# Optimization experiments

Hardware: AMD Instinct MI355X
Metric: run time of the kernel (lower is better)

The kernel has to match this reference:

```python
import jax, jax.numpy as jnp
import numpy as np

N_NODES = 50000
N_EDGES = 800000
C = 16          # in = hidden = out channels
FE = 8          # num_edge_features
NUM_GRAPHS = 64


def _nnconv(x, src, dst, edge_attr, w_e, b_e, root, bias):
    # edge MLP -> per-edge weight matrix [E, Cin, Cout]
    cin = x.shape[1]
    W = (edge_attr @ w_e + b_e).reshape(-1, cin, root.shape[1])
    msg = jnp.einsum('ei,eio->eo', x[src], W)            # gather + per-edge matvec
    n = x.shape[0]
    agg = jax.ops.segment_sum(msg, dst, num_segments=n)  # scatter-add
    cnt = jax.ops.segment_sum(jnp.ones((msg.shape[0], 1), x.dtype), dst, num_segments=n)
    agg = agg / jnp.maximum(cnt, 1.0)                    # aggr='mean'
    return x @ root + agg + bias


def setup_inputs() -> dict:
    key = jax.random.key(0)
    ks = jax.random.split(key, 12)
    x = jax.random.normal(ks[0], (N_NODES, C), dtype=jnp.float32)
    edge_index = jax.random.randint(ks[1], (2, N_EDGES), 0, N_NODES, dtype=jnp.int64)
    edge_attr = jax.random.uniform(ks[2], (N_EDGES, FE), dtype=jnp.float32)
    batch = jnp.sort(jax.random.randint(ks[3], (N_NODES,), 0, NUM_GRAPHS, dtype=jnp.int64))
    s = 1.0 / np.sqrt(C)
    se = 1.0 / np.sqrt(FE)
    we1 = jax.random.normal(ks[4], (FE, C * C), dtype=jnp.float32) * se
    be1 = jnp.zeros((C * C,), dtype=jnp.float32)
    root1 = jax.random.normal(ks[5], (C, C), dtype=jnp.float32) * s
    bias1 = jnp.zeros((C,), dtype=jnp.float32)
    we2 = jax.random.normal(ks[6], (FE, C * C), dtype=jnp.float32) * se
    be2 = jnp.zeros((C * C,), dtype=jnp.float32)
    root2 = jax.random.normal(ks[7], (C, C), dtype=jnp.float32) * s
    bias2 = jnp.zeros((C,), dtype=jnp.float32)
    return {"x": x, "edge_index": edge_index, "edge_attr": edge_attr, "batch": batch,
            "we1": we1, "be1": be1, "root1": root1, "bias1": bias1,
            "we2": we2, "be2": be2, "root2": root2, "bias2": bias2}


def reference(x, edge_index, edge_attr, batch,
              we1, be1, root1, bias1, we2, be2, root2, bias2):
    src, dst = edge_index[0], edge_index[1]
    # layer 1 (activation=None -> identity; dropout_prob=0 -> identity)
    h = _nnconv(x, src, dst, edge_attr, we1, be1, root1, bias1)
    # layer 2
    h = _nnconv(h, src, dst, edge_attr, we2, be2, root2, bias2)
    # global mean pool per graph, then flatten
    sums = jax.ops.segment_sum(h, batch, num_segments=NUM_GRAPHS)
    cnts = jax.ops.segment_sum(jnp.ones((h.shape[0], 1), h.dtype), batch, num_segments=NUM_GRAPHS)
    pooled = sums / jnp.maximum(cnts, 1.0)
    return pooled.reshape(-1)
```

## Files before the change

### kernel.cpp

```cpp
#include <hip/hip_runtime.h>

#define NN 50000
#define NE 800000
#define NG 64
#define NB ((NN + 255) / 256)
#define WSTR 164

__global__ __launch_bounds__(256) void histk(const int* __restrict__ dst,
                                             int* __restrict__ deg) {
    int e = blockIdx.x * 256 + threadIdx.x;
    if (e < NE) atomicAdd(&deg[dst[e]], 1);
}

__global__ __launch_bounds__(256) void bsumk(const int* __restrict__ deg,
                                             int* __restrict__ bsum) {
    int idx = blockIdx.x * 256 + threadIdx.x;
    int v = (idx < NN) ? deg[idx] : 0;
#pragma unroll
    for (int off = 32; off > 0; off >>= 1) v += __shfl_down(v, off);
    __shared__ int ws[4];
    int lane = threadIdx.x & 63, w = threadIdx.x >> 6;
    if (lane == 0) ws[w] = v;
    __syncthreads();
    if (threadIdx.x == 0) bsum[blockIdx.x] = ws[0] + ws[1] + ws[2] + ws[3];
}

__global__ __launch_bounds__(256) void bscank(const int* __restrict__ bsum,
                                              int* __restrict__ boffs) {
    int tid = threadIdx.x;
    int v = (tid < NB) ? bsum[tid] : 0;
    int lane = tid & 63, w = tid >> 6;
    int t = v;
#pragma unroll
    for (int off = 1; off < 64; off <<= 1) {
        int u = __shfl_up(t, off);
        if (lane >= off) t += u;
    }
    __shared__ int ws[4];
    if (lane == 63) ws[w] = t;
    __syncthreads();
    int add = 0;
    for (int k = 0; k < w; k++) add += ws[k];
    if (tid < NB) boffs[tid] = add + t - v;
}

__global__ __launch_bounds__(256) void fscank(const int* __restrict__ deg,
                                              const int* __restrict__ boffs,
                                              int* __restrict__ row,
                                              int* __restrict__ cur) {
    int idx = blockIdx.x * 256 + threadIdx.x;
    int v = (idx < NN) ? deg[idx] : 0;
    int lane = threadIdx.x & 63, w = threadIdx.x >> 6;
    int t = v;
#pragma unroll
    for (int off = 1; off < 64; off <<= 1) {
        int u = __shfl_up(t, off);
        if (lane >= off) t += u;
    }
    __shared__ int ws[4];
    if (lane == 63) ws[w] = t;
    __syncthreads();
    int add = boffs[blockIdx.x];
    for (int k = 0; k < w; k++) add += ws[k];
    int ex = add + t - v;
    if (idx < NN) { row[idx] = ex; cur[idx] = ex; }
    else if (idx == NN) row[NN] = ex;
}

__global__ __launch_bounds__(256) void scatk(const int* __restrict__ src,
                                             const int* __restrict__ dst,
                                             const float* __restrict__ ea,
                                             int* __restrict__ cur,
                                             float* __restrict__ rec) {
    int e = blockIdx.x * 256 + threadIdx.x;
    if (e >= NE) return;
    int d = dst[e];
    int pos = atomicAdd(&cur[d], 1);
    float4 a = *(const float4*)(ea + (size_t)e * 8);
    float4 b = *(const float4*)(ea + (size_t)e * 8 + 4);
    float4* r = (float4*)(rec + (size_t)pos * 16);
    float4 r0; r0.x = __int_as_float(src[e]); r0.y = a.x; r0.z = a.y; r0.w = a.z;
    float4 r1; r1.x = a.w; r1.y = b.x; r1.z = b.y; r1.w = b.z;
    float4 r2; r2.x = b.w; r2.y = 0.f; r2.z = 0.f; r2.w = 0.f;
    float4 r3; r3.x = 0.f; r3.y = 0.f; r3.z = 0.f; r3.w = 0.f;
    r[0] = r0; r[1] = r1; r[2] = r2; r[3] = r3;
}

template <bool POOL>
__global__ __launch_bounds__(256) void fusedk(const float* __restrict__ xin,
                                              const int* __restrict__ row,
                                              const float* __restrict__ rec,
                                              const float* __restrict__ we,
                                              const float* __restrict__ be,
                                              const float* __restrict__ root,
                                              const float* __restrict__ bias,
                                              const int* __restrict__ batch,
                                              float* __restrict__ out,
                                              float* __restrict__ gsum,
                                              float* __restrict__ gcnt) {
    __shared__ float wt[16 * WSTR];
    __shared__ float pls[16][WSTR];
    __shared__ float bs[16];
    __shared__ float gacc[16][16];
    __shared__ int gcnta[16];
    int tid = threadIdx.x;
    for (int idx = tid; idx < 2048; idx += 256) {
        int f = idx >> 8; int i = (idx >> 4) & 15; int o = idx & 15;
        wt[o * WSTR + f * 16 + i] = we[idx];
    }
    {
        int i = tid >> 4, o = tid & 15;
        wt[o * WSTR + 128 + i] = be[tid];
        wt[o * WSTR + 144 + i] = root[tid];
    }
    if (tid < 16) bs[tid] = bias[tid];
    if (POOL) {
        gacc[tid >> 4][tid & 15] = 0.f;
        if (tid < 16) gcnta[tid] = 0;
    }

    int g = tid >> 4, t = tid & 15;
    int v = blockIdx.x * 16 + g;
    int r0 = row[v], r1 = row[v + 1];

    float p0 = 0.f, p1 = 0.f, p2 = 0.f, p3 = 0.f;
    float p4 = 0.f, p5 = 0.f, p6 = 0.f, p7 = 0.f, s = 0.f;

    int pos = r0;
    int pend = r0 + ((r1 - r0) & ~3);
    for (; pos < pend; pos += 4) {
        const float* q0 = rec + (size_t)(pos + 0) * 16;
        const float* q1 = rec + (size_t)(pos + 1) * 16;
        const float* q2 = rec + (size_t)(pos + 2) * 16;
        const float* q3 = rec + (size_t)(pos + 3) * 16;
        float4 a0 = *(const float4*)q0; float4 b0 = *(const float4*)(q0 + 4); float e0 = q0[8];
        float4 a1 = *(const float4*)q1; float4 b1 = *(const float4*)(q1 + 4); float e1 = q1[8];
        float4 a2 = *(const float4*)q2; float4 b2 = *(const float4*)(q2 + 4); float e2 = q2[8];
        float4 a3 = *(const float4*)q3; float4 b3 = *(const float4*)(q3 + 4); float e3 = q3[8];
        float x0 = xin[(size_t)__float_as_int(a0.x) * 16 + t];
        float x1 = xin[(size_t)__float_as_int(a1.x) * 16 + t];
        float x2 = xin[(size_t)__float_as_int(a2.x) * 16 + t];
        float x3 = xin[(size_t)__float_as_int(a3.x) * 16 + t];
        p0 += a0.y * x0; p1 += a0.z * x0; p2 += a0.w * x0; p3 += b0.x * x0;
        p4 += b0.y * x0; p5 += b0.z * x0; p6 += b0.w * x0; p7 += e0 * x0; s += x0;
        p0 += a1.y * x1; p1 += a1.z * x1; p2 += a1.w * x1; p3 += b1.x * x1;
        p4 += b1.y * x1; p5 += b1.z * x1; p6 += b1.w * x1; p7 += e1 * x1; s += x1;
        p0 += a2.y * x2; p1 += a2.z * x2; p2 += a2.w * x2; p3 += b2.x * x2;
        p4 += b2.y * x2; p5 += b2.z * x2; p6 += b2.w * x2; p7 += e2 * x2; s += x2;
        p0 += a3.y * x3; p1 += a3.z * x3; p2 += a3.w * x3; p3 += b3.x * x3;
        p4 += b3.y * x3; p5 += b3.z * x3; p6 += b3.w * x3; p7 += e3 * x3; s += x3;
    }
    for (; pos < r1; ++pos) {
        const float* q = rec + (size_t)pos * 16;
        float4 a = *(const float4*)q; float4 b = *(const float4*)(q + 4); float e8 = q[8];
        float xv = xin[(size_t)__float_as_int(a.x) * 16 + t];
        p0 += a.y * xv; p1 += a.z * xv; p2 += a.w * xv; p3 += b.x * xv;
        p4 += b.y * xv; p5 += b.z * xv; p6 += b.w * xv; p7 += e8 * xv; s += xv;
    }

    pls[g][0 * 16 + t] = p0; pls[g][1 * 16 + t] = p1;
    pls[g][2 * 16 + t] = p2; pls[g][3 * 16 + t] = p3;
    pls[g][4 * 16 + t] = p4; pls[g][5 * 16 + t] = p5;
    pls[g][6 * 16 + t] = p6; pls[g][7 * 16 + t] = p7;
    pls[g][128 + t] = s;
    pls[g][144 + t] = xin[(size_t)v * 16 + t];
    __syncthreads();

    int o = t;
    const float4* pv = (const float4*)pls[g];
    const float4* wc = (const float4*)(wt + o * WSTR);
    float agg = 0.f;
#pragma unroll
    for (int k = 0; k < 36; k++) {
        float4 a = pv[k]; float4 wv = wc[k];
        agg += a.x * wv.x + a.y * wv.y + a.z * wv.z + a.w * wv.w;
    }
    float r = 0.f;
#pragma unroll
    for (int k = 36; k < 40; k++) {
        float4 a = pv[k]; float4 wv = wc[k];
        r += a.x * wv.x + a.y * wv.y + a.z * wv.z + a.w * wv.w;
    }
    int dg = r1 - r0;
    float h = r + agg / (float)(dg > 1 ? dg : 1) + bs[o];

    if (!POOL) {
        out[(size_t)v * 16 + o] = h;
    } else {
        int bmin = batch[blockIdx.x * 16];
        int b = batch[v];
        int slot = b - bmin;
        if (slot < 16) {
            atomicAdd(&gacc[slot][o], h);
            if (o == 0) atomicAdd(&gcnta[slot], 1);
        } else {
            atomicAdd(&gsum[(size_t)b * 16 + o], h);
            if (o == 0) atomicAdd(&gcnt[b], 1.0f);
        }
        __syncthreads();
        if (gcnta[g] > 0) {
            atomicAdd(&gsum[(size_t)(bmin + g) * 16 + o], gacc[g][o]);
            if (o == 0) atomicAdd(&gcnt[bmin + g], (float)gcnta[g]);
        }
    }
}

__global__ void fink(const float* __restrict__ gsum,
                     const float* __restrict__ gcnt,
                     float* __restrict__ out) {
    int i = blockIdx.x * 256 + threadIdx.x;
    if (i < NG * 16) out[i] = gsum[i] / fmaxf(gcnt[i >> 4], 1.0f);
}

extern "C" void kernel_launch(void* const* d_in, const int* in_sizes, int n_in,
                              void* d_out, int out_size, void* d_ws, size_t ws_size,
                              hipStream_t stream) {
    const float* x     = (const float*)d_in[0];
    const int*   ei    = (const int*)d_in[1];
    const float* ea    = (const float*)d_in[2];
    const int*   batch = (const int*)d_in[3];
    const float* we1   = (const float*)d_in[4];
    const float* be1   = (const float*)d_in[5];
    const float* root1 = (const float*)d_in[6];
    const float* bias1 = (const float*)d_in[7];
    const float* we2   = (const float*)d_in[8];
    const float* be2   = (const float*)d_in[9];
    const float* root2 = (const float*)d_in[10];
    const float* bias2 = (const float*)d_in[11];

    float* ws = (float*)d_ws;
    float* rec  = ws;
    float* h1   = rec + (size_t)NE * 16;
    int*   row  = (int*)(h1 + (size_t)NN * 16);
    int*   cur  = row + NN + 1;
    int*   deg  = cur + NN;
    int*   bsum = deg + NN;
    int*   boffs= bsum + NB;
    float* gsum = (float*)(boffs + NB);
    float* gcnt = gsum + NG * 16;

    hipMemsetAsync(deg, 0, (size_t)(NN + 2 * NB + NG * 16 + NG) * 4, stream);

    const int* src = ei;
    const int* dst = ei + NE;

    int gE = (NE + 255) / 256;
    int gV = NN / 16;

    histk<<<gE, 256, 0, stream>>>(dst, deg);
    bsumk<<<NB, 256, 0, stream>>>(deg, bsum);
    bscank<<<1, 256, 0, stream>>>(bsum, boffs);
    fscank<<<NB, 256, 0, stream>>>(deg, boffs, row, cur);
    scatk<<<gE, 256, 0, stream>>>(src, dst, ea, cur, rec);

    fusedk<false><<<gV, 256, 0, stream>>>(x, row, rec, we1, be1, root1, bias1,
                                          batch, h1, gsum, gcnt);
    fusedk<true><<<gV, 256, 0, stream>>>(h1, row, rec, we2, be2, root2, bias2,
                                         batch, h1 , gsum, gcnt);

    fink<<<4, 256, 0, stream>>>(gsum, gcnt, (float*)d_out);
}
```

Before: 184.9 us.

## Replace LDS staging of partial sums with register matvec and shuffle reduction

Each thread now keeps its per-input-channel partials in registers and computes contributions to all 16 outputs from a reorganized weight layout in LDS. A recursive-halving butterfly of xor shuffles reduces these across the 16 lanes of a node group, so the pls shared buffer and its store/load round trip are gone. A single sync now sits after the weight load, replacing the one that came before the matvec. The cost is a 16-element register array and more shuffle instructions, which may raise register pressure.

```diff
diff --git a/kernel.cpp b/kernel.cpp
--- a/kernel.cpp
+++ b/kernel.cpp
@@ -4,7 +4,7 @@
 #define NE 800000
 #define NG 64
 #define NB ((NN + 255) / 256)
-#define WSTR 164
+#define WROW 193
 
 __global__ __launch_bounds__(256) void histk(const int* __restrict__ dst,
                                              int* __restrict__ deg) {
@@ -98,26 +98,26 @@
                                               float* __restrict__ out,
                                               float* __restrict__ gsum,
                                               float* __restrict__ gcnt) {
-    __shared__ float wt[16 * WSTR];
-    __shared__ float pls[16][WSTR];
+    __shared__ float wlds[16 * WROW];
     __shared__ float bs[16];
     __shared__ float gacc[16][16];
     __shared__ int gcnta[16];
     int tid = threadIdx.x;
     for (int idx = tid; idx < 2048; idx += 256) {
-        int f = idx >> 8; int i = (idx >> 4) & 15; int o = idx & 15;
-        wt[o * WSTR + f * 16 + i] = we[idx];
+        int f = idx >> 8, rest = idx & 255, i = rest >> 4, o = rest & 15;
+        wlds[i * WROW + o * 12 + f] = we[idx];
     }
     {
         int i = tid >> 4, o = tid & 15;
-        wt[o * WSTR + 128 + i] = be[tid];
-        wt[o * WSTR + 144 + i] = root[tid];
+        wlds[i * WROW + o * 12 + 8] = be[tid];
+        wlds[i * WROW + o * 12 + 9] = root[tid];
     }
     if (tid < 16) bs[tid] = bias[tid];
     if (POOL) {
         gacc[tid >> 4][tid & 15] = 0.f;
         if (tid < 16) gcnta[tid] = 0;
     }
+    __syncthreads();
 
     int g = tid >> 4, t = tid & 15;
     int v = blockIdx.x * 16 + g;
@@ -158,49 +158,68 @@
         p4 += b.y * xv; p5 += b.z * xv; p6 += b.w * xv; p7 += e8 * xv; s += xv;
     }
 
-    pls[g][0 * 16 + t] = p0; pls[g][1 * 16 + t] = p1;
-    pls[g][2 * 16 + t] = p2; pls[g][3 * 16 + t] = p3;
-    pls[g][4 * 16 + t] = p4; pls[g][5 * 16 + t] = p5;
-    pls[g][6 * 16 + t] = p6; pls[g][7 * 16 + t] = p7;
-    pls[g][128 + t] = s;
-    pls[g][144 + t] = xin[(size_t)v * 16 + t];
-    __syncthreads();
-
-    int o = t;
-    const float4* pv = (const float4*)pls[g];
-    const float4* wc = (const float4*)(wt + o * WSTR);
-    float agg = 0.f;
-#pragma unroll
-    for (int k = 0; k < 36; k++) {
-        float4 a = pv[k]; float4 wv = wc[k];
-        agg += a.x * wv.x + a.y * wv.y + a.z * wv.z + a.w * wv.w;
-    }
-    float r = 0.f;
-#pragma unroll
-    for (int k = 36; k < 40; k++) {
-        float4 a = pv[k]; float4 wv = wc[k];
-        r += a.x * wv.x + a.y * wv.y + a.z * wv.z + a.w * wv.w;
-    }
     int dg = r1 - r0;
-    float h = r + agg / (float)(dg > 1 ? dg : 1) + bs[o];
+    float inv = 1.0f / (float)(dg > 1 ? dg : 1);
+    float xv = xin[(size_t)v * 16 + t];
+
+    float a[16];
+    const float* wr = wlds + t * WROW;
+#pragma unroll
+    for (int o = 0; o < 16; o++) {
+        const float* w = wr + o * 12;
+        float agg = w[0] * p0 + w[1] * p1 + w[2] * p2 + w[3] * p3 +
+                    w[4] * p4 + w[5] * p5 + w[6] * p6 + w[7] * p7 + w[8] * s;
+        a[o] = agg * inv + w[9] * xv;
+    }
+
+    {
+        int bit = (t >> 3) & 1;
+#pragma unroll
+        for (int k = 0; k < 8; k++) {
+            float snd = bit ? a[k] : a[k + 8];
+            float kp  = bit ? a[k + 8] : a[k];
+            a[k] = kp + __shfl_xor(snd, 8);
+        }
+        bit = (t >> 2) & 1;
+#pragma unroll
+        for (int k = 0; k < 4; k++) {
+            float snd = bit ? a[k] : a[k + 4];
+            float kp  = bit ? a[k + 4] : a[k];
+            a[k] = kp + __shfl_xor(snd, 4);
+        }
+        bit = (t >> 1) & 1;
+#pragma unroll
+        for (int k = 0; k < 2; k++) {
+            float snd = bit ? a[k] : a[k + 2];
+            float kp  = bit ? a[k + 2] : a[k];
+            a[k] = kp + __shfl_xor(snd, 2);
+        }
+        bit = t & 1;
+        {
+            float snd = bit ? a[0] : a[1];
+            float kp  = bit ? a[1] : a[0];
+            a[0] = kp + __shfl_xor(snd, 1);
+        }
+    }
+    float h = a[0] + bs[t];
 
     if (!POOL) {
-        out[(size_t)v * 16 + o] = h;
+        out[(size_t)v * 16 + t] = h;
     } else {
         int bmin = batch[blockIdx.x * 16];
         int b = batch[v];
         int slot = b - bmin;
         if (slot < 16) {
-            atomicAdd(&gacc[slot][o], h);
-            if (o == 0) atomicAdd(&gcnta[slot], 1);
+            atomicAdd(&gacc[slot][t], h);
+            if (t == 0) atomicAdd(&gcnta[slot], 1);
         } else {
-            atomicAdd(&gsum[(size_t)b * 16 + o], h);
-            if (o == 0) atomicAdd(&gcnt[b], 1.0f);
+            atomicAdd(&gsum[(size_t)b * 16 + t], h);
+            if (t == 0) atomicAdd(&gcnt[b], 1.0f);
         }
         __syncthreads();
         if (gcnta[g] > 0) {
-            atomicAdd(&gsum[(size_t)(bmin + g) * 16 + o], gacc[g][o]);
-            if (o == 0) atomicAdd(&gcnt[bmin + g], (float)gcnta[g]);
+            atomicAdd(&gsum[(size_t)(bmin + g) * 16 + t], gacc[g][t]);
+            if (t == 0) atomicAdd(&gcnt[bmin + g], (float)gcnta[g]);
         }
     }
 }
```

Measured after the change: 190.4 us. 1.03x slower.
